# Performance work log

Hardware: AMD Instinct MI355X
Metric: run time of the kernel (lower is better)

## Reference

```python
import jax, jax.numpy as jnp
import numpy as np

BN_EPS = 1e-3  # keras BatchNormalization default epsilon


def setup_inputs() -> dict:
    key = jax.random.key(0)
    ks = jax.random.split(key, 12)
    B, K, F = 32, 1024, 16
    H, C = 64, 4
    inp = {
        "x": jax.random.normal(ks[0], (B, K, F), dtype=jnp.float32),
        "coordinates": jax.random.normal(ks[1], (B, K, 3), dtype=jnp.float32),
        "precision_squared": jax.random.uniform(ks[2], (1,), dtype=jnp.float32),
        # dense kernels (no dense bias in the original; scalar per-block bias instead)
        "W0": 0.05 * jax.random.normal(ks[3], (2 * F, H), dtype=jnp.float32),
        "W1": 0.05 * jax.random.normal(ks[4], (4 * H, H), dtype=jnp.float32),
        "W2": 0.05 * jax.random.normal(ks[5], (4 * H, H), dtype=jnp.float32),
        "W3": 0.05 * jax.random.normal(ks[6], (4 * H, C), dtype=jnp.float32),
        "b0": 0.05 * jax.random.normal(ks[7], (1,), dtype=jnp.float32),
        "b1": 0.05 * jax.random.normal(ks[8], (1,), dtype=jnp.float32),
        "b2": 0.05 * jax.random.normal(ks[9], (1,), dtype=jnp.float32),
        "b3": 0.05 * jax.random.normal(ks[10], (1,), dtype=jnp.float32),
        # batchnorm affine params (inference mode, moving_mean=0, moving_var=1)
        "g0": jnp.ones((H,), jnp.float32), "be0": jnp.zeros((H,), jnp.float32),
        "g1": jnp.ones((H,), jnp.float32), "be1": jnp.zeros((H,), jnp.float32),
        "g2": jnp.ones((H,), jnp.float32), "be2": jnp.zeros((H,), jnp.float32),
    }
    return inp


def _adjacency(coordinates, precision_squared):
    # pairwise squared distances per sample: [B,K,K]
    norms = jnp.sum(coordinates * coordinates, axis=-1)  # [B,K]
    dist = norms[:, :, None] - 2.0 * jnp.einsum("bkd,bjd->bkj", coordinates, coordinates) + norms[:, None, :]
    A = jnp.exp(-dist * precision_squared[0])
    return jax.nn.softmax(A, axis=-1)  # per-sample axis=1 == last axis of [K,K]


def _block(x, A, W, b, gamma, beta, final):
    h = jnp.einsum("bij,bjf->bif", A, x)          # matmul(A, x)
    h = jnp.concatenate([h, x], axis=-1) @ W + b[0]
    if not final:
        # inference BN with moving_mean=0, moving_var=1
        h = h * (gamma / jnp.sqrt(1.0 + BN_EPS)) + beta
        h = jnp.concatenate([h, jax.nn.relu(h)], axis=-1)
    return h


def reference(x, coordinates, precision_squared, W0, W1, W2, W3,
              b0, b1, b2, b3, g0, be0, g1, be1, g2, be2):
    A = _adjacency(coordinates, precision_squared)
    h = _block(x, A, W0, b0, g0, be0, False)
    h = _block(h, A, W1, b1, g1, be1, False)
    h = _block(h, A, W2, b2, g2, be2, False)
    h = _block(h, A, W3, b3, None, None, True)   # final block: no BN, no activation
    h = jnp.mean(h, axis=1)                      # [B, num_classes]
    return jax.nn.softmax(h, axis=1)
```

## Files before the change

kernel.cpp:

```cpp
#include <hip/hip_runtime.h>
#include <math.h>

typedef __attribute__((ext_vector_type(8)))  __bf16   bf16x8;
typedef __attribute__((ext_vector_type(4)))  float    f32x4;
typedef __attribute__((ext_vector_type(16))) float    f32x16;
typedef __attribute__((ext_vector_type(4)))  unsigned u32x4;
typedef __attribute__((ext_vector_type(2)))  unsigned u32x2;

__device__ __forceinline__ unsigned short f2bf(float f) {
    unsigned u = __builtin_bit_cast(unsigned, f);
    u += 0x7fffu + ((u >> 16) & 1u);
    return (unsigned short)(u >> 16);
}
__device__ __forceinline__ float bf2f(unsigned short b) {
    unsigned u = ((unsigned)b) << 16;
    return __builtin_bit_cast(float, u);
}
__device__ __forceinline__ unsigned swz3(int key) { return (unsigned)((key ^ (key >> 3)) & 7); }
__device__ __forceinline__ bf16x8 ldfrag(const char* p) { return __builtin_bit_cast(bf16x8, *(const u32x4*)p); }

__global__ __launch_bounds__(256)
void wconv(const float* __restrict__ W0, const float* __restrict__ W1,
           const float* __restrict__ W2, const float* __restrict__ W3,
           unsigned short* __restrict__ wt)
{
    int id = blockIdx.x * 256 + threadIdx.x;
    if (id >= 51200) return;
    float v; size_t dst;
    if (id < 2048)       { int h = id >> 5, f = id & 31;              v = W0[f*64 + h]; dst = (size_t)h*32 + f; }
    else if (id < 18432) { int j = id - 2048;  int h = j >> 8, f = j & 255; v = W1[f*64 + h]; dst = 2048  + (size_t)h*256 + f; }
    else if (id < 34816) { int j = id - 18432; int h = j >> 8, f = j & 255; v = W2[f*64 + h]; dst = 18432 + (size_t)h*256 + f; }
    else                 { int j = id - 34816; int h = j >> 8, f = j & 255; v = (h < 4) ? W3[f*4 + h] : 0.f; dst = 34816 + (size_t)h*256 + f; }
    wt[dst] = f2bf(v);
}

__global__ __launch_bounds__(256)
void x0conv(const float* __restrict__ x, unsigned short* __restrict__ xT0,
            unsigned short* __restrict__ xR0)
{
    int id = blockIdx.x * 256 + threadIdx.x;
    int b = id >> 10, j = id & 1023;
    const float* s = x + (size_t)id * 16;
    unsigned pk[8];
#pragma unroll
    for (int f = 0; f < 16; f += 2) {
        unsigned short h0 = f2bf(s[f]);
        unsigned short h1 = f2bf(s[f + 1]);
        xT0[((size_t)b*16 + f    )*1024 + j] = h0;
        xT0[((size_t)b*16 + f + 1)*1024 + j] = h1;
        pk[f >> 1] = (unsigned)h0 | ((unsigned)h1 << 16);
    }
    u32x4* d = (u32x4*)(xR0 + (size_t)id * 16);
    u32x4 v0 = {pk[0], pk[1], pk[2], pk[3]};
    u32x4 v1 = {pk[4], pk[5], pk[6], pk[7]};
    d[0] = v0; d[1] = v1;
}

template<int MODE>
__global__ __launch_bounds__(256, 2)
void gcn_block(const unsigned short* __restrict__ xT, const unsigned short* __restrict__ xR,
               const float* __restrict__ coords, const float* __restrict__ psq,
               const unsigned short* __restrict__ WThi,
               const float* __restrict__ gamma, const float* __restrict__ beta,
               const float* __restrict__ bias,
               unsigned short* __restrict__ Tg, float* __restrict__ RinvG,
               unsigned short* __restrict__ oxT, unsigned short* __restrict__ oxR,
               float* __restrict__ part)
{
    __shared__ char smem[65536];
    constexpr int XTO = 0;
    constexpr int THI = 16 * 1024;
    constexpr int SC4 = 32 * 1024;
    constexpr int C0O = 0;
    constexpr int W0H = 4 * 1024;
    constexpr int RED = SC4;
    constexpr int RIV = SC4 + 1024;
    constexpr int XTB  = 0;
    constexpr int TTB  = 32 * 1024;
    constexpr int RIVM = 48 * 1024;
    constexpr int YL   = 0;
    constexpr int XI   = 16 * 1024;
    constexpr int WTB  = 32 * 1024;
    constexpr int SPT  = 48 * 1024 + 512;
    constexpr int ZT   = 0;

    const int t = threadIdx.x;
    const int l = t & 63;
    const int w = t >> 6;
    const int b  = blockIdx.y;
    const int it = blockIdx.x;
    const int i0g = it * 64;
    const int m31 = l & 31, kg = l >> 5;
    const int m15 = l & 15, kg4 = l >> 4;
    const int wf = w >> 1, wi = w & 1;
    float bv = 0.f;
    if constexpr (MODE != 2) bv = bias[0];

    int fA0 = 0, fA1 = 0, iB = 0;
    if constexpr (MODE) { fA0 = wf*64 + m31; fA1 = fA0 + 32; iB = wi*32 + m31; }
    else                { fA0 = m15;                          iB = w*16 + m15; }

    f32x16 acc0, acc1; f32x4 acc4;
#pragma unroll
    for (int r = 0; r < 16; ++r) { acc0[r] = 0.f; acc1[r] = 0.f; }
#pragma unroll
    for (int r = 0; r < 4; ++r) acc4[r] = 0.f;

    if constexpr (MODE == 0) {
        const float p = psq[0];
        float4* sc = (float4*)(smem + SC4);
        for (int k = t; k < 1024; k += 256) {
            const float* c = coords + ((size_t)b * 1024 + k) * 3;
            float cx = c[0], cy = c[1], cz = c[2];
            sc[k] = make_float4(cx, cy, cz, cx*cx + cy*cy + cz*cz);
        }
        __syncthreads();
        const float4 ci = sc[i0g + l];
        float rsum = 0.f;

        for (int jt = 0; jt < 16; ++jt) {
            __syncthreads();
            if (t < 128) {
                const int f = t >> 3, g8 = t & 7;
                const unsigned short* g = xT + ((size_t)b*16 + f)*1024 + jt*64 + g8*8;
                u32x4 v = *(const u32x4*)g;
                *(u32x4*)(smem + XTO + f*128 + ((g8*16) ^ (swz3(f) << 4))) = v;
            }
            {
                const int j0 = jt*64 + w*16;
                unsigned hp[8];
#pragma unroll
                for (int q = 0; q < 8; ++q) {
                    float4 cj0 = sc[j0 + 2*q], cj1 = sc[j0 + 2*q + 1];
                    float d0 = ci.w + cj0.w - 2.f*(ci.x*cj0.x + ci.y*cj0.y + ci.z*cj0.z);
                    float d1 = ci.w + cj1.w - 2.f*(ci.x*cj1.x + ci.y*cj1.y + ci.z*cj1.z);
                    unsigned short h0 = f2bf(__expf(__expf(-d0 * p)));
                    unsigned short h1 = f2bf(__expf(__expf(-d1 * p)));
                    rsum += bf2f(h0) + bf2f(h1);
                    hp[q] = (unsigned)h0 | ((unsigned)h1 << 16);
                }
                const unsigned sw = swz3(l) << 4;
                char* th = smem + THI + l*128;
                u32x4 a = {hp[0], hp[1], hp[2], hp[3]}, c2 = {hp[4], hp[5], hp[6], hp[7]};
                *(u32x4*)(th + ((w*32 +  0) ^ sw)) = a;
                *(u32x4*)(th + ((w*32 + 16) ^ sw)) = c2;
            }
            __syncthreads();
            {
                const int r = t >> 2, c = t & 3;
                const char* th = smem + THI + r*128;
                const unsigned swr = swz3(r) << 4;
                u32x4 v0 = *(const u32x4*)(th + ((c*32     ) ^ swr));
                u32x4 v1 = *(const u32x4*)(th + ((c*32 + 16) ^ swr));
                unsigned short* dT = Tg + ((size_t)(b*1024 + i0g + r))*1024 + jt*64 + c*16;
                *(u32x4*)dT = v0;
                *(u32x4*)(dT + 8) = v1;
            }
            {
                const char* rA  = smem + XTO + fA0*128; const unsigned sA = swz3(fA0) << 4;
                const char* rBh = smem + THI + iB*128;  const unsigned sB = swz3(iB) << 4;
#pragma unroll
                for (int kk = 0; kk < 2; ++kk) {
                    const unsigned off = kk*64 + kg4*16;
                    bf16x8 a  = ldfrag(rA  + (off ^ sA));
                    bf16x8 bh = ldfrag(rBh + (off ^ sB));
                    acc4 = __builtin_amdgcn_mfma_f32_16x16x32_bf16(a, bh, acc4, 0, 0, 0);
                }
            }
        }
        __syncthreads();
        ((float*)(smem + RED))[w*64 + l] = rsum;
        __syncthreads();
        if (t < 64) {
            const float* rr = (const float*)(smem + RED);
            float s = rr[t] + rr[64 + t] + rr[128 + t] + rr[192 + t];
            float rv = 1.f / s;
            ((float*)(smem + RIV))[t] = rv;
            RinvG[(size_t)b*1024 + i0g + t] = rv;
        }
        __syncthreads();
    } else {
        if (t < 64) ((float*)(smem + RIVM))[t] = RinvG[(size_t)b*1024 + i0g + t];
        const int sf = t >> 1, shf = t & 1;
        const int sti = t >> 2, stc = t & 3;
        const unsigned short* gxb = xT + ((size_t)b*128 + sf)*1024 + shf*32;
        const unsigned short* gtb = Tg + ((size_t)(b*1024 + i0g + sti))*1024 + stc*16;
        u32x4 rx0, rx1, rx2, rx3, rt0, rt1;
        rx0 = *(const u32x4*)(gxb);      rx1 = *(const u32x4*)(gxb + 8);
        rx2 = *(const u32x4*)(gxb + 16); rx3 = *(const u32x4*)(gxb + 24);
        rt0 = *(const u32x4*)(gtb);      rt1 = *(const u32x4*)(gtb + 8);

        const unsigned swx = swz3(sf) << 4;
        const unsigned swt = swz3(sti) << 4;
        const unsigned sA0 = swz3(fA0) << 4;
        const unsigned sA1 = swz3(fA1) << 4;
        const unsigned sB  = swz3(iB) << 4;

        for (int jt = 0; jt < 16; ++jt) {
            const int p = jt & 1;
            {
                char* xrow = smem + XTB + p*16384 + sf*128;
                *(u32x4*)(xrow + ((shf*64 +  0) ^ swx)) = rx0;
                *(u32x4*)(xrow + ((shf*64 + 16) ^ swx)) = rx1;
                *(u32x4*)(xrow + ((shf*64 + 32) ^ swx)) = rx2;
                *(u32x4*)(xrow + ((shf*64 + 48) ^ swx)) = rx3;
                char* trow = smem + TTB + p*8192 + sti*128;
                *(u32x4*)(trow + ((stc*32     ) ^ swt)) = rt0;
                *(u32x4*)(trow + ((stc*32 + 16) ^ swt)) = rt1;
            }
            if (jt < 15) {
                const unsigned short* g = gxb + (jt + 1)*64;
                rx0 = *(const u32x4*)(g);      rx1 = *(const u32x4*)(g + 8);
                rx2 = *(const u32x4*)(g + 16); rx3 = *(const u32x4*)(g + 24);
                const unsigned short* gT = gtb + (jt + 1)*64;
                rt0 = *(const u32x4*)(gT);     rt1 = *(const u32x4*)(gT + 8);
            }
            __syncthreads();
            const char* rA0 = smem + XTB + p*16384 + fA0*128;
            const char* rA1 = smem + XTB + p*16384 + fA1*128;
            const char* rBh = smem + TTB + p*8192  + iB*128;
#pragma unroll
            for (int kk = 0; kk < 4; ++kk) {
                const unsigned off = kk*32 + kg*16;
                bf16x8 a0 = ldfrag(rA0 + (off ^ sA0));
                bf16x8 a1 = ldfrag(rA1 + (off ^ sA1));
                bf16x8 bh = ldfrag(rBh + (off ^ sB));
                acc0 = __builtin_amdgcn_mfma_f32_32x32x16_bf16(a0, bh, acc0, 0, 0, 0);
                acc1 = __builtin_amdgcn_mfma_f32_32x32x16_bf16(a1, bh, acc1, 0, 0, 0);
            }
        }
        __syncthreads();
    }

    if constexpr (MODE) {
        const float rv = ((const float*)(smem + RIVM))[iB];
        acc0 *= rv; acc1 *= rv;
        char* yrow = smem + YL + iB*256;
        const unsigned swi = swz3(iB) << 4;
#pragma unroll
        for (int rq = 0; rq < 4; ++rq) {
            unsigned q0 = (unsigned)f2bf(acc0[rq*4+0]) | ((unsigned)f2bf(acc0[rq*4+1]) << 16);
            unsigned q1 = (unsigned)f2bf(acc0[rq*4+2]) | ((unsigned)f2bf(acc0[rq*4+3]) << 16);
            u32x2 w0 = {q0, q1};
            *(u32x2*)(yrow + ((wf*128 + rq*16 + kg*8) ^ swi)) = w0;
            unsigned r0 = (unsigned)f2bf(acc1[rq*4+0]) | ((unsigned)f2bf(acc1[rq*4+1]) << 16);
            unsigned r1 = (unsigned)f2bf(acc1[rq*4+2]) | ((unsigned)f2bf(acc1[rq*4+3]) << 16);
            u32x2 w1 = {r0, r1};
            *(u32x2*)(yrow + ((wf*128 + 64 + rq*16 + kg*8) ^ swi)) = w1;
        }
        const int xi_i = t >> 2, xq = t & 3;
        const unsigned short* gx = xR + ((size_t)(b*1024 + i0g + xi_i))*128 + xq*32;
        char* xrow = smem + XI + xi_i*256;
        const unsigned swxi = swz3(xi_i) << 4;
#pragma unroll
        for (int g = 0; g < 4; ++g) {
            u32x4 v = *(const u32x4*)(gx + g*8);
            *(u32x4*)(xrow + ((xq*64 + g*16) ^ swxi)) = v;
        }
        {
            const int h = t >> 2, q = t & 3;
            const unsigned short* gw = WThi + h*256 + q*32;
            char* wrow = smem + WTB + h*256;
            const unsigned sw = swz3(h) << 4;
#pragma unroll
            for (int g = 0; g < 4; ++g) {
                u32x4 v = *(const u32x4*)(gw + g*8);
                *(u32x4*)(wrow + ((q*64 + g*16) ^ sw)) = v;
            }
        }
    } else {
        const float rv = ((const float*)(smem + RIV))[iB];
        acc4 *= rv;
        unsigned q0 = (unsigned)f2bf(acc4[0]) | ((unsigned)f2bf(acc4[1]) << 16);
        unsigned q1 = (unsigned)f2bf(acc4[2]) | ((unsigned)f2bf(acc4[3]) << 16);
        u32x2 w0 = {q0, q1};
        *(u32x2*)(smem + C0O + iB*64 + ((kg4*8) ^ ((swz3(iB) & 3) << 4))) = w0;
        const int xi_i = t >> 2, xq = t & 3;
        const unsigned short* gx = xR + ((size_t)(b*1024 + i0g + xi_i))*16 + xq*4;
        u32x2 v = *(const u32x2*)gx;
        *(u32x2*)(smem + C0O + xi_i*64 + ((32 + xq*8) ^ ((swz3(xi_i) & 3) << 4))) = v;
    }
    __syncthreads();

    f32x16 dacc; f32x4 da0, da1, da2, da3;
#pragma unroll
    for (int r = 0; r < 16; ++r) dacc[r] = bv;
#pragma unroll
    for (int r = 0; r < 4; ++r) { da0[r] = bv; da1[r] = bv; da2[r] = bv; da3[r] = bv; }

    if constexpr (MODE) {
        const int hA = wf*32 + m31;
        const char* rWh = smem + WTB + hA*256;  const unsigned sH = swz3(hA) << 4;
        const char* rBY = smem + YL + iB*256;   const unsigned sI = swz3(iB) << 4;
#pragma unroll
        for (int k8 = 0; k8 < 8; ++k8) {
            const unsigned off = k8*32 + kg*16;
            bf16x8 ah = ldfrag(rWh + (off ^ sH));
            bf16x8 bb = ldfrag(rBY + (off ^ sI));
            dacc = __builtin_amdgcn_mfma_f32_32x32x16_bf16(ah, bb, dacc, 0, 0, 0);
        }
        __syncthreads();
        {
            const int h = t >> 2, q = t & 3;
            const unsigned short* gw = WThi + h*256 + 128 + q*32;
            char* wrow = smem + WTB + h*256;
            const unsigned sw = swz3(h) << 4;
#pragma unroll
            for (int g = 0; g < 4; ++g) {
                u32x4 v = *(const u32x4*)(gw + g*8);
                *(u32x4*)(wrow + ((q*64 + g*16) ^ sw)) = v;
            }
        }
        __syncthreads();
        const char* rBX = smem + XI + iB*256;
#pragma unroll
        for (int k8 = 0; k8 < 8; ++k8) {
            const unsigned off = k8*32 + kg*16;
            bf16x8 ah = ldfrag(rWh + (off ^ sH));
            bf16x8 bb = ldfrag(rBX + (off ^ sI));
            dacc = __builtin_amdgcn_mfma_f32_32x32x16_bf16(ah, bb, dacc, 0, 0, 0);
        }
        __syncthreads();
    } else {
        {
            if (t < 128) {
                const int h = t >> 1, hf = t & 1;
                const unsigned short* gw = WThi + h*32 + hf*16;
                char* wrow = smem + W0H + h*64;
                const unsigned sw2 = (swz3(h) & 3) << 4;
#pragma unroll
                for (int g = 0; g < 2; ++g) {
                    u32x4 v = *(const u32x4*)(gw + g*8);
                    *(u32x4*)(wrow + (((hf*2 + g)*16) ^ sw2)) = v;
                }
            }
        }
        __syncthreads();
        const int hA = w*16 + m15;
        const unsigned sH2 = (swz3(hA) & 3) << 4;
        bf16x8 ah = ldfrag(smem + W0H + hA*64 + ((kg4*16) ^ sH2));
        {
            const int i0 = m15;
            bf16x8 b0 = ldfrag(smem + C0O + (i0     )*64 + ((kg4*16) ^ ((swz3(i0     ) & 3) << 4)));
            bf16x8 b1 = ldfrag(smem + C0O + (i0 + 16)*64 + ((kg4*16) ^ ((swz3(i0 + 16) & 3) << 4)));
            bf16x8 b2 = ldfrag(smem + C0O + (i0 + 32)*64 + ((kg4*16) ^ ((swz3(i0 + 32) & 3) << 4)));
            bf16x8 b3 = ldfrag(smem + C0O + (i0 + 48)*64 + ((kg4*16) ^ ((swz3(i0 + 48) & 3) << 4)));
            da0 = __builtin_amdgcn_mfma_f32_16x16x32_bf16(ah, b0, da0, 0, 0, 0);
            da1 = __builtin_amdgcn_mfma_f32_16x16x32_bf16(ah, b1, da1, 0, 0, 0);
            da2 = __builtin_amdgcn_mfma_f32_16x16x32_bf16(ah, b2, da2, 0, 0, 0);
            da3 = __builtin_amdgcn_mfma_f32_16x16x32_bf16(ah, b3, da3, 0, 0, 0);
        }
        __syncthreads();
    }

    float* zt = (float*)(smem + ZT);
    if constexpr (MODE == 2) {
        if (wf == 0) {
#pragma unroll
            for (int r = 0; r < 4; ++r) {
                float v = dacc[r];
                v += __shfl_xor(v, 1);  v += __shfl_xor(v, 2);  v += __shfl_xor(v, 4);
                v += __shfl_xor(v, 8);  v += __shfl_xor(v, 16);
                if (l == 0) ((float*)(smem + SPT))[w*4 + r] = v;
            }
        }
        __syncthreads();
        if (t < 4) {
            const float* sp = (const float*)(smem + SPT);
            part[((size_t)b*16 + it)*4 + t] = sp[t] + sp[4 + t];
        }
        return;
    } else {
        const float bns = rsqrtf(1.f + 1e-3f);
        if constexpr (MODE) {
#pragma unroll
            for (int r = 0; r < 16; ++r) {
                const int h = wf*32 + (r & 3) + 8*(r >> 2) + 4*kg;
                zt[h*65 + iB] = dacc[r] * (gamma[h] * bns) + beta[h];
            }
        } else {
#pragma unroll
            for (int r = 0; r < 4; ++r) {
                const int h = w*16 + kg4*4 + r;
                const float gs = gamma[h] * bns, bt = beta[h];
                zt[h*65 + (m15     )] = da0[r] * gs + bt;
                zt[h*65 + (m15 + 16)] = da1[r] * gs + bt;
                zt[h*65 + (m15 + 32)] = da2[r] * gs + bt;
                zt[h*65 + (m15 + 48)] = da3[r] * gs + bt;
            }
        }
        __syncthreads();
        {
            const int h = t & 63, ic = (t >> 6) * 16;
            const float* zr = zt + h*65 + ic;
            unsigned pz[8], pr[8];
#pragma unroll
            for (int q = 0; q < 8; ++q) {
                float z0 = zr[2*q], z1 = zr[2*q + 1];
                pz[q] = (unsigned)f2bf(z0) | ((unsigned)f2bf(z1) << 16);
                pr[q] = (unsigned)f2bf(fmaxf(z0, 0.f)) | ((unsigned)f2bf(fmaxf(z1, 0.f)) << 16);
            }
            unsigned short* d0 = oxT + ((size_t)b*128 + h     )*1024 + i0g + ic;
            unsigned short* d1 = oxT + ((size_t)b*128 + h + 64)*1024 + i0g + ic;
            u32x4 a = {pz[0], pz[1], pz[2], pz[3]}, c = {pz[4], pz[5], pz[6], pz[7]};
            u32x4 e = {pr[0], pr[1], pr[2], pr[3]}, f = {pr[4], pr[5], pr[6], pr[7]};
            *(u32x4*)(d0) = a; *(u32x4*)(d0 + 8) = c;
            *(u32x4*)(d1) = e; *(u32x4*)(d1 + 8) = f;
        }
        {
            const int i = t >> 2, fq = t & 3;
            unsigned pk[16];
#pragma unroll
            for (int ff = 0; ff < 16; ++ff) {
                const int f0 = fq*32 + ff*2, f1 = f0 + 1;
                float v0 = (f0 < 64) ? zt[f0*65 + i] : fmaxf(zt[(f0 - 64)*65 + i], 0.f);
                float v1 = (f1 < 64) ? zt[f1*65 + i] : fmaxf(zt[(f1 - 64)*65 + i], 0.f);
                pk[ff] = (unsigned)f2bf(v0) | ((unsigned)f2bf(v1) << 16);
            }
            unsigned short* d = oxR + ((size_t)(b*1024 + i0g + i))*128 + fq*32;
            u32x4 a = {pk[0],  pk[1],  pk[2],  pk[3]};
            u32x4 c = {pk[4],  pk[5],  pk[6],  pk[7]};
            u32x4 e = {pk[8],  pk[9],  pk[10], pk[11]};
            u32x4 f = {pk[12], pk[13], pk[14], pk[15]};
            *(u32x4*)(d)      = a; *(u32x4*)(d + 8)  = c;
            *(u32x4*)(d + 16) = e; *(u32x4*)(d + 24) = f;
        }
    }
}

__global__ void finalize_kernel(const float* __restrict__ part, const float* __restrict__ b3,
                                float* __restrict__ out)
{
    const int b = threadIdx.x;
    if (b < 32) {
        float v[4] = {0.f, 0.f, 0.f, 0.f};
        for (int i = 0; i < 16; ++i)
#pragma unroll
            for (int h = 0; h < 4; ++h) v[h] += part[((size_t)b*16 + i)*4 + h];
        const float bb = b3[0];
#pragma unroll
        for (int h = 0; h < 4; ++h) v[h] = v[h] * (1.f / 1024.f) + bb;
        const float m = fmaxf(fmaxf(v[0], v[1]), fmaxf(v[2], v[3]));
        float e[4], se = 0.f;
#pragma unroll
        for (int h = 0; h < 4; ++h) { e[h] = __expf(v[h] - m); se += e[h]; }
        const float inv = 1.f / se;
#pragma unroll
        for (int h = 0; h < 4; ++h) out[b*4 + h] = e[h] * inv;
    }
}

extern "C" void kernel_launch(void* const* d_in, const int* in_sizes, int n_in,
                              void* d_out, int out_size, void* d_ws, size_t ws_size,
                              hipStream_t stream)
{
    const float* x   = (const float*)d_in[0];
    const float* co  = (const float*)d_in[1];
    const float* psq = (const float*)d_in[2];
    const float* W0  = (const float*)d_in[3];
    const float* W1  = (const float*)d_in[4];
    const float* W2  = (const float*)d_in[5];
    const float* W3  = (const float*)d_in[6];
    const float* b0  = (const float*)d_in[7];
    const float* b1  = (const float*)d_in[8];
    const float* b2  = (const float*)d_in[9];
    const float* b3  = (const float*)d_in[10];
    const float* g0  = (const float*)d_in[11];
    const float* be0 = (const float*)d_in[12];
    const float* g1  = (const float*)d_in[13];
    const float* be1 = (const float*)d_in[14];
    const float* g2  = (const float*)d_in[15];
    const float* be2 = (const float*)d_in[16];

    char* ws = (char*)d_ws;
    const size_t MB = (size_t)1 << 20;
    unsigned short* Tg  = (unsigned short*)(ws);
    unsigned short* xTa = (unsigned short*)(ws + 64*MB);
    unsigned short* xRa = (unsigned short*)(ws + 72*MB);
    unsigned short* xTb = (unsigned short*)(ws + 80*MB);
    unsigned short* xRb = (unsigned short*)(ws + 88*MB);
    unsigned short* xT0 = (unsigned short*)(ws + 96*MB);
    unsigned short* xR0 = (unsigned short*)(ws + 97*MB);
    unsigned short* wt  = (unsigned short*)(ws + 98*MB);
    float* RinvG        = (float*)(ws + 98*MB + 256*1024);
    float* part         = (float*)(ws + 98*MB + 512*1024);

    unsigned short* WT0 = wt;
    unsigned short* WT1 = wt + 2048;
    unsigned short* WT2 = wt + 18432;
    unsigned short* WT3 = wt + 34816;

    wconv<<<dim3(200), 256, 0, stream>>>(W0, W1, W2, W3, wt);
    x0conv<<<dim3(128), 256, 0, stream>>>(x, xT0, xR0);

    dim3 grid(16, 32);
    gcn_block<0><<<grid, 256, 0, stream>>>(xT0, xR0, co, psq, WT0, g0, be0, b0, Tg, RinvG, xTa, xRa, nullptr);
    gcn_block<1><<<grid, 256, 0, stream>>>(xTa, xRa, nullptr, nullptr, WT1, g1, be1, b1, Tg, RinvG, xTb, xRb, nullptr);
    gcn_block<1><<<grid, 256, 0, stream>>>(xTb, xRb, nullptr, nullptr, WT2, g2, be2, b2, Tg, RinvG, xTa, xRa, nullptr);
    gcn_block<2><<<grid, 256, 0, stream>>>(xTa, xRa, nullptr, nullptr, WT3, nullptr, nullptr, nullptr, Tg, RinvG,
                                           nullptr, nullptr, part);
    finalize_kernel<<<1, 64, 0, stream>>>(part, b3, (float*)d_out);
}
```

Baseline: 204.3 us.

## Split adjacency generation into separate normalized kernel and merge prep kernels

Moves the softmax-adjacency computation out of the first GCN block into a dedicated tgen kernel that computes row sums in registers and writes a pre-normalized bf16 adjacency matrix. Each block then reads the normalized matrix and no longer needs RinvG or a rescale. Block 0 becomes a double-buffered streaming matmul with smaller shared memory, and occupancy hints go up. The two preprocessing kernels are merged into one launch. The cost is an extra kernel and a second bf16 rounding of the adjacency values (normalizing already-rounded entries).

```diff
diff --git a/kernel.cpp b/kernel.cpp
--- a/kernel.cpp
+++ b/kernel.cpp
@@ -20,68 +20,120 @@
 __device__ __forceinline__ bf16x8 ldfrag(const char* p) { return __builtin_bit_cast(bf16x8, *(const u32x4*)p); }
 
 __global__ __launch_bounds__(256)
-void wconv(const float* __restrict__ W0, const float* __restrict__ W1,
-           const float* __restrict__ W2, const float* __restrict__ W3,
-           unsigned short* __restrict__ wt)
+void prep(const float* __restrict__ W0, const float* __restrict__ W1,
+          const float* __restrict__ W2, const float* __restrict__ W3,
+          const float* __restrict__ x,
+          unsigned short* __restrict__ wt,
+          unsigned short* __restrict__ xT0, unsigned short* __restrict__ xR0)
 {
-    int id = blockIdx.x * 256 + threadIdx.x;
-    if (id >= 51200) return;
-    float v; size_t dst;
-    if (id < 2048)       { int h = id >> 5, f = id & 31;              v = W0[f*64 + h]; dst = (size_t)h*32 + f; }
-    else if (id < 18432) { int j = id - 2048;  int h = j >> 8, f = j & 255; v = W1[f*64 + h]; dst = 2048  + (size_t)h*256 + f; }
-    else if (id < 34816) { int j = id - 18432; int h = j >> 8, f = j & 255; v = W2[f*64 + h]; dst = 18432 + (size_t)h*256 + f; }
-    else                 { int j = id - 34816; int h = j >> 8, f = j & 255; v = (h < 4) ? W3[f*4 + h] : 0.f; dst = 34816 + (size_t)h*256 + f; }
-    wt[dst] = f2bf(v);
-}
-
-__global__ __launch_bounds__(256)
-void x0conv(const float* __restrict__ x, unsigned short* __restrict__ xT0,
-            unsigned short* __restrict__ xR0)
+    const int blk = blockIdx.x, t = threadIdx.x;
+    if (blk < 200) {
+        int id = blk * 256 + t;
+        if (id >= 51200) return;
+        float v; size_t dst;
+        if (id < 2048)       { int h = id >> 5, f = id & 31;              v = W0[f*64 + h]; dst = (size_t)h*32 + f; }
+        else if (id < 18432) { int j = id - 2048;  int h = j >> 8, f = j & 255; v = W1[f*64 + h]; dst = 2048  + (size_t)h*256 + f; }
+        else if (id < 34816) { int j = id - 18432; int h = j >> 8, f = j & 255; v = W2[f*64 + h]; dst = 18432 + (size_t)h*256 + f; }
+        else                 { int j = id - 34816; int h = j >> 8, f = j & 255; v = (h < 4) ? W3[f*4 + h] : 0.f; dst = 34816 + (size_t)h*256 + f; }
+        wt[dst] = f2bf(v);
+    } else {
+        int id = (blk - 200) * 256 + t;
+        int b = id >> 10, j = id & 1023;
+        const float* s = x + (size_t)id * 16;
+        unsigned pk[8];
+#pragma unroll
+        for (int f = 0; f < 16; f += 2) {
+            unsigned short h0 = f2bf(s[f]);
+            unsigned short h1 = f2bf(s[f + 1]);
+            xT0[((size_t)b*16 + f    )*1024 + j] = h0;
+            xT0[((size_t)b*16 + f + 1)*1024 + j] = h1;
+            pk[f >> 1] = (unsigned)h0 | ((unsigned)h1 << 16);
+        }
+        u32x4* d = (u32x4*)(xR0 + (size_t)id * 16);
+        u32x4 v0 = {pk[0], pk[1], pk[2], pk[3]};
+        u32x4 v1 = {pk[4], pk[5], pk[6], pk[7]};
+        d[0] = v0; d[1] = v1;
+    }
+}
+
+__global__ __launch_bounds__(256, 4)
+void tgen(const float* __restrict__ coords, const float* __restrict__ psq,
+          unsigned short* __restrict__ Tg)
 {
-    int id = blockIdx.x * 256 + threadIdx.x;
-    int b = id >> 10, j = id & 1023;
-    const float* s = x + (size_t)id * 16;
-    unsigned pk[8];
-#pragma unroll
-    for (int f = 0; f < 16; f += 2) {
-        unsigned short h0 = f2bf(s[f]);
-        unsigned short h1 = f2bf(s[f + 1]);
-        xT0[((size_t)b*16 + f    )*1024 + j] = h0;
-        xT0[((size_t)b*16 + f + 1)*1024 + j] = h1;
-        pk[f >> 1] = (unsigned)h0 | ((unsigned)h1 << 16);
-    }
-    u32x4* d = (u32x4*)(xR0 + (size_t)id * 16);
-    u32x4 v0 = {pk[0], pk[1], pk[2], pk[3]};
-    u32x4 v1 = {pk[4], pk[5], pk[6], pk[7]};
-    d[0] = v0; d[1] = v1;
+    __shared__ float4 sc[1024];
+    const int t = threadIdx.x;
+    const int b = blockIdx.y;
+    const int i0 = blockIdx.x * 16;
+    for (int k = t; k < 1024; k += 256) {
+        const float* c = coords + ((size_t)b*1024 + k)*3;
+        float cx = c[0], cy = c[1], cz = c[2];
+        sc[k] = make_float4(cx, cy, cz, cx*cx + cy*cy + cz*cz);
+    }
+    __syncthreads();
+    const float p = psq[0];
+    const int r = t >> 4, jg = t & 15;
+    const float4 ci = sc[i0 + r];
+    u32x4 pk0, pk1, pk2, pk3, pk4, pk5, pk6, pk7;
+    u32x4* pk[8] = {&pk0,&pk1,&pk2,&pk3,&pk4,&pk5,&pk6,&pk7};
+    float rsum = 0.f;
+#pragma unroll
+    for (int pp = 0; pp < 8; ++pp) {
+        const int jb = pp*128 + jg*8;
+        u32x4 v;
+#pragma unroll
+        for (int e = 0; e < 4; ++e) {
+            float4 cj0 = sc[jb + 2*e], cj1 = sc[jb + 2*e + 1];
+            float d0 = ci.w + cj0.w - 2.f*(ci.x*cj0.x + ci.y*cj0.y + ci.z*cj0.z);
+            float d1 = ci.w + cj1.w - 2.f*(ci.x*cj1.x + ci.y*cj1.y + ci.z*cj1.z);
+            unsigned short h0 = f2bf(__expf(__expf(-d0 * p)));
+            unsigned short h1 = f2bf(__expf(__expf(-d1 * p)));
+            rsum += bf2f(h0) + bf2f(h1);
+            v[e] = (unsigned)h0 | ((unsigned)h1 << 16);
+        }
+        *pk[pp] = v;
+    }
+    rsum += __shfl_xor(rsum, 1);
+    rsum += __shfl_xor(rsum, 2);
+    rsum += __shfl_xor(rsum, 4);
+    rsum += __shfl_xor(rsum, 8);
+    const float rinv = 1.f / rsum;
+    unsigned short* dst = Tg + ((size_t)(b*1024 + i0 + r))*1024;
+#pragma unroll
+    for (int pp = 0; pp < 8; ++pp) {
+        u32x4 u = *pk[pp], v;
+#pragma unroll
+        for (int e = 0; e < 4; ++e) {
+            unsigned uu = u[e];
+            float lo = bf2f((unsigned short)(uu & 0xffffu)) * rinv;
+            float hi = bf2f((unsigned short)(uu >> 16)) * rinv;
+            v[e] = (unsigned)f2bf(lo) | ((unsigned)f2bf(hi) << 16);
+        }
+        *(u32x4*)(dst + pp*128 + jg*8) = v;
+    }
 }
 
 template<int MODE>
-__global__ __launch_bounds__(256, 2)
+__global__ __launch_bounds__(256, MODE ? 3 : 4)
 void gcn_block(const unsigned short* __restrict__ xT, const unsigned short* __restrict__ xR,
-               const float* __restrict__ coords, const float* __restrict__ psq,
+               const unsigned short* __restrict__ Tg,
                const unsigned short* __restrict__ WThi,
                const float* __restrict__ gamma, const float* __restrict__ beta,
                const float* __restrict__ bias,
-               unsigned short* __restrict__ Tg, float* __restrict__ RinvG,
                unsigned short* __restrict__ oxT, unsigned short* __restrict__ oxR,
                float* __restrict__ part)
 {
-    __shared__ char smem[65536];
-    constexpr int XTO = 0;
-    constexpr int THI = 16 * 1024;
-    constexpr int SC4 = 32 * 1024;
-    constexpr int C0O = 0;
-    constexpr int W0H = 4 * 1024;
-    constexpr int RED = SC4;
-    constexpr int RIV = SC4 + 1024;
+    constexpr int SMEM = MODE ? 49664 : 20480;
+    __shared__ char smem[SMEM];
     constexpr int XTB  = 0;
     constexpr int TTB  = 32 * 1024;
-    constexpr int RIVM = 48 * 1024;
+    constexpr int SPT  = 49152;
     constexpr int YL   = 0;
     constexpr int XI   = 16 * 1024;
     constexpr int WTB  = 32 * 1024;
-    constexpr int SPT  = 48 * 1024 + 512;
+    constexpr int XT0B = 0;
+    constexpr int TT0B = 4096;
+    constexpr int C0O  = 0;
+    constexpr int W0H  = 4096;
     constexpr int ZT   = 0;
 
     const int t = threadIdx.x;
@@ -106,95 +158,22 @@
 #pragma unroll
     for (int r = 0; r < 4; ++r) acc4[r] = 0.f;
 
-    if constexpr (MODE == 0) {
-        const float p = psq[0];
-        float4* sc = (float4*)(smem + SC4);
-        for (int k = t; k < 1024; k += 256) {
-            const float* c = coords + ((size_t)b * 1024 + k) * 3;
-            float cx = c[0], cy = c[1], cz = c[2];
-            sc[k] = make_float4(cx, cy, cz, cx*cx + cy*cy + cz*cz);
-        }
-        __syncthreads();
-        const float4 ci = sc[i0g + l];
-        float rsum = 0.f;
-
-        for (int jt = 0; jt < 16; ++jt) {
-            __syncthreads();
-            if (t < 128) {
-                const int f = t >> 3, g8 = t & 7;
-                const unsigned short* g = xT + ((size_t)b*16 + f)*1024 + jt*64 + g8*8;
-                u32x4 v = *(const u32x4*)g;
-                *(u32x4*)(smem + XTO + f*128 + ((g8*16) ^ (swz3(f) << 4))) = v;
-            }
-            {
-                const int j0 = jt*64 + w*16;
-                unsigned hp[8];
-#pragma unroll
-                for (int q = 0; q < 8; ++q) {
-                    float4 cj0 = sc[j0 + 2*q], cj1 = sc[j0 + 2*q + 1];
-                    float d0 = ci.w + cj0.w - 2.f*(ci.x*cj0.x + ci.y*cj0.y + ci.z*cj0.z);
-                    float d1 = ci.w + cj1.w - 2.f*(ci.x*cj1.x + ci.y*cj1.y + ci.z*cj1.z);
-                    unsigned short h0 = f2bf(__expf(__expf(-d0 * p)));
-                    unsigned short h1 = f2bf(__expf(__expf(-d1 * p)));
-                    rsum += bf2f(h0) + bf2f(h1);
-                    hp[q] = (unsigned)h0 | ((unsigned)h1 << 16);
-                }
-                const unsigned sw = swz3(l) << 4;
-                char* th = smem + THI + l*128;
-                u32x4 a = {hp[0], hp[1], hp[2], hp[3]}, c2 = {hp[4], hp[5], hp[6], hp[7]};
-                *(u32x4*)(th + ((w*32 +  0) ^ sw)) = a;
-                *(u32x4*)(th + ((w*32 + 16) ^ sw)) = c2;
-            }
-            __syncthreads();
-            {
-                const int r = t >> 2, c = t & 3;
-                const char* th = smem + THI + r*128;
-                const unsigned swr = swz3(r) << 4;
-                u32x4 v0 = *(const u32x4*)(th + ((c*32     ) ^ swr));
-                u32x4 v1 = *(const u32x4*)(th + ((c*32 + 16) ^ swr));
-                unsigned short* dT = Tg + ((size_t)(b*1024 + i0g + r))*1024 + jt*64 + c*16;
-                *(u32x4*)dT = v0;
-                *(u32x4*)(dT + 8) = v1;
-            }
-            {
-                const char* rA  = smem + XTO + fA0*128; const unsigned sA = swz3(fA0) << 4;
-                const char* rBh = smem + THI + iB*128;  const unsigned sB = swz3(iB) << 4;
-#pragma unroll
-                for (int kk = 0; kk < 2; ++kk) {
-                    const unsigned off = kk*64 + kg4*16;
-                    bf16x8 a  = ldfrag(rA  + (off ^ sA));
-                    bf16x8 bh = ldfrag(rBh + (off ^ sB));
-                    acc4 = __builtin_amdgcn_mfma_f32_16x16x32_bf16(a, bh, acc4, 0, 0, 0);
-                }
-            }
-        }
-        __syncthreads();
-        ((float*)(smem + RED))[w*64 + l] = rsum;
-        __syncthreads();
-        if (t < 64) {
-            const float* rr = (const float*)(smem + RED);
-            float s = rr[t] + rr[64 + t] + rr[128 + t] + rr[192 + t];
-            float rv = 1.f / s;
-            ((float*)(smem + RIV))[t] = rv;
-            RinvG[(size_t)b*1024 + i0g + t] = rv;
-        }
-        __syncthreads();
-    } else {
-        if (t < 64) ((float*)(smem + RIVM))[t] = RinvG[(size_t)b*1024 + i0g + t];
+    const int sti = t >> 2, stc = t & 3;
+    const unsigned short* gtb = Tg + ((size_t)(b*1024 + i0g + sti))*1024 + stc*16;
+    u32x4 rt0 = *(const u32x4*)(gtb);
+    u32x4 rt1 = *(const u32x4*)(gtb + 8);
+    const unsigned swt = swz3(sti) << 4;
+    const unsigned sB  = swz3(iB) << 4;
+
+    if constexpr (MODE) {
         const int sf = t >> 1, shf = t & 1;
-        const int sti = t >> 2, stc = t & 3;
         const unsigned short* gxb = xT + ((size_t)b*128 + sf)*1024 + shf*32;
-        const unsigned short* gtb = Tg + ((size_t)(b*1024 + i0g + sti))*1024 + stc*16;
-        u32x4 rx0, rx1, rx2, rx3, rt0, rt1;
+        u32x4 rx0, rx1, rx2, rx3;
         rx0 = *(const u32x4*)(gxb);      rx1 = *(const u32x4*)(gxb + 8);
         rx2 = *(const u32x4*)(gxb + 16); rx3 = *(const u32x4*)(gxb + 24);
-        rt0 = *(const u32x4*)(gtb);      rt1 = *(const u32x4*)(gtb + 8);
-
         const unsigned swx = swz3(sf) << 4;
-        const unsigned swt = swz3(sti) << 4;
         const unsigned sA0 = swz3(fA0) << 4;
         const unsigned sA1 = swz3(fA1) << 4;
-        const unsigned sB  = swz3(iB) << 4;
 
         for (int jt = 0; jt < 16; ++jt) {
             const int p = jt & 1;
@@ -229,12 +208,43 @@
                 acc1 = __builtin_amdgcn_mfma_f32_32x32x16_bf16(a1, bh, acc1, 0, 0, 0);
             }
         }
-        __syncthreads();
-    }
+    } else {
+        const int sf0 = t >> 3, sc8 = t & 7;
+        const unsigned short* gxb = xT + ((size_t)b*16 + sf0)*1024 + sc8*8;
+        u32x4 rxa = {0,0,0,0};
+        if (t < 128) rxa = *(const u32x4*)gxb;
+        const unsigned swx0 = swz3(sf0) << 4;
+        const unsigned sA = swz3(fA0) << 4;
+
+        for (int jt = 0; jt < 16; ++jt) {
+            const int p = jt & 1;
+            if (t < 128)
+                *(u32x4*)(smem + XT0B + p*2048 + sf0*128 + ((sc8*16) ^ swx0)) = rxa;
+            {
+                char* trow = smem + TT0B + p*8192 + sti*128;
+                *(u32x4*)(trow + ((stc*32     ) ^ swt)) = rt0;
+                *(u32x4*)(trow + ((stc*32 + 16) ^ swt)) = rt1;
+            }
+            if (jt < 15) {
+                if (t < 128) rxa = *(const u32x4*)(gxb + (jt + 1)*64);
+                const unsigned short* gT = gtb + (jt + 1)*64;
+                rt0 = *(const u32x4*)(gT);  rt1 = *(const u32x4*)(gT + 8);
+            }
+            __syncthreads();
+            const char* rA  = smem + XT0B + p*2048 + fA0*128;
+            const char* rBh = smem + TT0B + p*8192 + iB*128;
+#pragma unroll
+            for (int kk = 0; kk < 2; ++kk) {
+                const unsigned off = kk*64 + kg4*16;
+                bf16x8 a  = ldfrag(rA  + (off ^ sA));
+                bf16x8 bh = ldfrag(rBh + (off ^ sB));
+                acc4 = __builtin_amdgcn_mfma_f32_16x16x32_bf16(a, bh, acc4, 0, 0, 0);
+            }
+        }
+    }
+    __syncthreads();
 
     if constexpr (MODE) {
-        const float rv = ((const float*)(smem + RIVM))[iB];
-        acc0 *= rv; acc1 *= rv;
         char* yrow = smem + YL + iB*256;
         const unsigned swi = swz3(iB) << 4;
 #pragma unroll
@@ -269,8 +279,6 @@
             }
         }
     } else {
-        const float rv = ((const float*)(smem + RIV))[iB];
-        acc4 *= rv;
         unsigned q0 = (unsigned)f2bf(acc4[0]) | ((unsigned)f2bf(acc4[1]) << 16);
         unsigned q1 = (unsigned)f2bf(acc4[2]) | ((unsigned)f2bf(acc4[3]) << 16);
         u32x2 w0 = {q0, q1};
@@ -279,6 +287,17 @@
         const unsigned short* gx = xR + ((size_t)(b*1024 + i0g + xi_i))*16 + xq*4;
         u32x2 v = *(const u32x2*)gx;
         *(u32x2*)(smem + C0O + xi_i*64 + ((32 + xq*8) ^ ((swz3(xi_i) & 3) << 4))) = v;
+        if (t < 128) {
+            const int h = t >> 1, hf = t & 1;
+            const unsigned short* gw = WThi + h*32 + hf*16;
+            char* wrow = smem + W0H + h*64;
+            const unsigned sw2 = (swz3(h) & 3) << 4;
+#pragma unroll
+            for (int g = 0; g < 2; ++g) {
+                u32x4 v2 = *(const u32x4*)(gw + g*8);
+                *(u32x4*)(wrow + (((hf*2 + g)*16) ^ sw2)) = v2;
+            }
+        }
     }
     __syncthreads();
 
@@ -322,20 +341,6 @@
         }
         __syncthreads();
     } else {
-        {
-            if (t < 128) {
-                const int h = t >> 1, hf = t & 1;
-                const unsigned short* gw = WThi + h*32 + hf*16;
-                char* wrow = smem + W0H + h*64;
-                const unsigned sw2 = (swz3(h) & 3) << 4;
-#pragma unroll
-                for (int g = 0; g < 2; ++g) {
-                    u32x4 v = *(const u32x4*)(gw + g*8);
-                    *(u32x4*)(wrow + (((hf*2 + g)*16) ^ sw2)) = v;
-                }
-            }
-        }
-        __syncthreads();
         const int hA = w*16 + m15;
         const unsigned sH2 = (swz3(hA) & 3) << 4;
         bf16x8 ah = ldfrag(smem + W0H + hA*64 + ((kg4*16) ^ sH2));
@@ -482,22 +487,21 @@
     unsigned short* xT0 = (unsigned short*)(ws + 96*MB);
     unsigned short* xR0 = (unsigned short*)(ws + 97*MB);
     unsigned short* wt  = (unsigned short*)(ws + 98*MB);
-    float* RinvG        = (float*)(ws + 98*MB + 256*1024);
-    float* part         = (float*)(ws + 98*MB + 512*1024);
+    float* part         = (float*)(ws + 98*MB + 256*1024);
 
     unsigned short* WT0 = wt;
     unsigned short* WT1 = wt + 2048;
     unsigned short* WT2 = wt + 18432;
     unsigned short* WT3 = wt + 34816;
 
-    wconv<<<dim3(200), 256, 0, stream>>>(W0, W1, W2, W3, wt);
-    x0conv<<<dim3(128), 256, 0, stream>>>(x, xT0, xR0);
+    prep<<<dim3(328), 256, 0, stream>>>(W0, W1, W2, W3, x, wt, xT0, xR0);
+    tgen<<<dim3(64, 32), 256, 0, stream>>>(co, psq, Tg);
 
     dim3 grid(16, 32);
-    gcn_block<0><<<grid, 256, 0, stream>>>(xT0, xR0, co, psq, WT0, g0, be0, b0, Tg, RinvG, xTa, xRa, nullptr);
-    gcn_block<1><<<grid, 256, 0, stream>>>(xTa, xRa, nullptr, nullptr, WT1, g1, be1, b1, Tg, RinvG, xTb, xRb, nullptr);
-    gcn_block<1><<<grid, 256, 0, stream>>>(xTb, xRb, nullptr, nullptr, WT2, g2, be2, b2, Tg, RinvG, xTa, xRa, nullptr);
-    gcn_block<2><<<grid, 256, 0, stream>>>(xTa, xRa, nullptr, nullptr, WT3, nullptr, nullptr, nullptr, Tg, RinvG,
+    gcn_block<0><<<grid, 256, 0, stream>>>(xT0, xR0, Tg, WT0, g0, be0, b0, xTa, xRa, nullptr);
+    gcn_block<1><<<grid, 256, 0, stream>>>(xTa, xRa, Tg, WT1, g1, be1, b1, xTb, xRb, nullptr);
+    gcn_block<1><<<grid, 256, 0, stream>>>(xTb, xRb, Tg, WT2, g2, be2, b2, xTa, xRa, nullptr);
+    gcn_block<2><<<grid, 256, 0, stream>>>(xTa, xRa, Tg, WT3, nullptr, nullptr, nullptr,
                                            nullptr, nullptr, part);
     finalize_kernel<<<1, 64, 0, stream>>>(part, b3, (float*)d_out);
 }
```

Result: slower. 221.0 us (+8.2%).
